# Kernel tuning notes

Measured on AMD Instinct MI355X. Metric: run time of the kernel, lower is better.

The kernel has to match this reference:

```python
import jax, jax.numpy as jnp
import numpy as np

B, T, D = 16, 512, 1024
H = 4
DH = D // H
L = 2
FF = 4 * D
MAX_CORR = 3
THRESH = 0.3
EPS = 1e-5


def _ln(x, g, b):
    mu = x.mean(-1, keepdims=True)
    var = ((x - mu) ** 2).mean(-1, keepdims=True)
    return (x - mu) / jnp.sqrt(var + EPS) * g + b


def _prm(x, Wqkv, bqkv, Wo, bo, ln1_g, ln1_b, W1, b1, W2, b2, ln2_g, ln2_b,
         rh_W1, rh_b1, rh_W2, rh_b2):
    # PyTorch TransformerEncoder (post-LN, relu, dropout off) with causal mask
    Bs, Ts, _ = x.shape
    causal = jnp.triu(jnp.ones((Ts, Ts), dtype=bool), k=1)  # True = masked
    for l in range(L):
        qkv = x @ Wqkv[l].T + bqkv[l]  # (B,T,3D)
        q, k, v = jnp.split(qkv, 3, axis=-1)
        q = q.reshape(Bs, Ts, H, DH)
        k = k.reshape(Bs, Ts, H, DH)
        v = v.reshape(Bs, Ts, H, DH)
        scores = jnp.einsum('bthd,bshd->bhts', q, k) / jnp.sqrt(jnp.float32(DH))
        scores = jnp.where(causal[None, None], -jnp.inf, scores)
        attn = jax.nn.softmax(scores, axis=-1)
        o = jnp.einsum('bhts,bshd->bthd', attn, v).reshape(Bs, Ts, D)
        o = o @ Wo[l].T + bo[l]
        x = _ln(x + o, ln1_g[l], ln1_b[l])
        h = jax.nn.relu(x @ W1[l].T + b1[l]) @ W2[l].T + b2[l]
        x = _ln(x + h, ln2_g[l], ln2_b[l])
    r = jax.nn.relu(x @ rh_W1.T + rh_b1) @ rh_W2.T + rh_b2  # (B,T,1)
    return jax.nn.sigmoid(r[..., 0])  # (B,T)


def setup_inputs() -> dict:
    key = jax.random.key(0)
    ks = jax.random.split(key, 24)
    s = 0.02
    inp = {
        'chain': jax.random.normal(ks[0], (B, T, D), jnp.float32),
        'Wqkv': jax.random.normal(ks[1], (L, 3 * D, D), jnp.float32) * s,
        'bqkv': jnp.zeros((L, 3 * D), jnp.float32),
        'Wo': jax.random.normal(ks[2], (L, D, D), jnp.float32) * s,
        'bo': jnp.zeros((L, D), jnp.float32),
        'ln1_g': jnp.ones((L, D), jnp.float32),
        'ln1_b': jnp.zeros((L, D), jnp.float32),
        'W1': jax.random.normal(ks[3], (L, FF, D), jnp.float32) * s,
        'b1': jnp.zeros((L, FF), jnp.float32),
        'W2': jax.random.normal(ks[4], (L, D, FF), jnp.float32) * s,
        'b2': jnp.zeros((L, D), jnp.float32),
        'ln2_g': jnp.ones((L, D), jnp.float32),
        'ln2_b': jnp.zeros((L, D), jnp.float32),
        'rh_W1': jax.random.normal(ks[5], (D // 2, D), jnp.float32) * s,
        'rh_b1': jnp.zeros((D // 2,), jnp.float32),
        'rh_W2': jax.random.normal(ks[6], (1, D // 2), jnp.float32) * s,
        'rh_b2': jnp.full((1,), -1.0, jnp.float32),  # bias so some scores fall below threshold
        'cor_W1': jax.random.normal(ks[7], (2 * D, 2 * D), jnp.float32) * s,
        'cor_b1': jnp.zeros((2 * D,), jnp.float32),
        'cor_W2': jax.random.normal(ks[8], (D, 2 * D), jnp.float32) * s,
        'cor_b2': jnp.zeros((D,), jnp.float32),
    }
    return inp


def reference(chain, Wqkv, bqkv, Wo, bo, ln1_g, ln1_b, W1, b1, W2, b2,
              ln2_g, ln2_b, rh_W1, rh_b1, rh_W2, rh_b2,
              cor_W1, cor_b1, cor_W2, cor_b2):
    prm = lambda x: _prm(x, Wqkv, bqkv, Wo, bo, ln1_g, ln1_b, W1, b1, W2, b2,
                         ln2_g, ln2_b, rh_W1, rh_b1, rh_W2, rh_b2)
    scores0 = prm(chain)
    corrected = chain
    counts = jnp.zeros((B,), jnp.int32)
    offs = jnp.array([-1, 0, 1], jnp.int32)
    tpos = jnp.arange(T)
    for _ in range(MAX_CORR):
        s = prm(corrected)  # (B,T)
        below = s < THRESH
        has_bad = below.any(axis=-1)  # (B,)
        # worst = first argmin among below-threshold steps (matches torch argmin over gathered)
        w = jnp.argmin(jnp.where(below, s, jnp.inf), axis=-1)  # (B,)
        # context: mean over valid window [w-1, w+2)
        idxs = w[:, None] + offs  # (B,3)
        valid = (idxs >= 0) & (idxs < T)
        gathered = jnp.take_along_axis(corrected, jnp.clip(idxs, 0, T - 1)[..., None], axis=1)  # (B,3,D)
        ctx = (gathered * valid[..., None]).sum(1) / valid.sum(1, keepdims=True)  # (B,D)
        cur = jnp.take_along_axis(corrected, jnp.broadcast_to(w[:, None, None], (B, 1, D)), axis=1)[:, 0]  # (B,D)
        cinp = jnp.concatenate([cur, ctx], axis=-1)  # (B,2D)
        new_step = jax.nn.relu(cinp @ cor_W1.T + cor_b1) @ cor_W2.T + cor_b2  # (B,D)
        sel = (tpos[None, :] == w[:, None]) & has_bad[:, None]  # (B,T)
        corrected = jnp.where(sel[..., None], new_step[:, None, :], corrected)
        counts = counts + has_bad.astype(jnp.int32)
    final_scores = prm(corrected)
    improved = final_scores.mean(-1) > scores0.mean(-1)
    return corrected, counts, final_scores, improved
```

## Files before the change

### kernel.cpp

```cpp
#include <hip/hip_runtime.h>
#include <math.h>

#define B_ 16
#define T_ 512
#define D_ 1024
#define H_ 4
#define DH_ 256
#define FF_ 4096
#define M_ (B_*T_)
#define THRESH_ 0.3f
#define EPS_ 1e-5f

#define GF_RELU 1
#define GF_RES  2
#define GF_OUTBF16 4
#define GF_SPLITV 8

typedef unsigned short ushort_t;
typedef unsigned int uint_t;

using s16x8 = __attribute__((ext_vector_type(8))) short;
using f32x4 = __attribute__((ext_vector_type(4))) float;

typedef const __attribute__((address_space(1))) void* gas_ptr;
typedef __attribute__((address_space(3))) void* lds_ptr;

static __device__ __forceinline__ ushort_t f2bf(float f) {
  uint_t x = __float_as_uint(f);
  return (ushort_t)((x + 0x7FFFu + ((x >> 16) & 1u)) >> 16);
}
static __device__ __forceinline__ float bf2f(ushort_t u) {
  return __uint_as_float(((uint_t)u) << 16);
}

__global__ __launch_bounds__(256)
void cvt_f32_bf16(const float* __restrict__ in, ushort_t* __restrict__ out, int n)
{
  const int i = (blockIdx.x * 256 + threadIdx.x) << 2;
  if (i >= n) return;
  const float4 v = *(const float4*)(in + i);
  ushort4 o;
  o.x = f2bf(v.x); o.y = f2bf(v.y); o.z = f2bf(v.z); o.w = f2bf(v.w);
  *(ushort4*)(out + i) = o;
}

__global__ __launch_bounds__(256)
void gemm_bf16(const ushort_t* __restrict__ A, const ushort_t* __restrict__ Bt,
               const float* __restrict__ bias, const ushort_t* __restrict__ res,
               float* __restrict__ outF, ushort_t* __restrict__ outB,
               ushort_t* __restrict__ vt,
               int M, int N, int K, int flags)
{
  __shared__ ushort_t As[128 * 32];
  __shared__ ushort_t Bs[128 * 32];
  const int n0 = blockIdx.x << 7;
  const int m0 = blockIdx.y << 7;
  const int tid = threadIdx.x;
  const int wv = tid >> 6, ln = tid & 63;
  const int wm = (wv >> 1) << 6;
  const int wn = (wv & 1) << 6;
  const int lrow = ln & 15, quad = ln >> 4;

  f32x4 acc[4][4] = {};

  const ushort_t* ga = A + (size_t)(m0 + wv * 16 + (ln >> 2)) * K + ((ln & 3) << 3);
  const ushort_t* gb = Bt + (size_t)(n0 + wv * 16 + (ln >> 2)) * K + ((ln & 3) << 3);
  ushort_t* lA = &As[wv * 512];
  ushort_t* lB = &Bs[wv * 512];

  for (int k0 = 0; k0 < K; k0 += 32) {
    __builtin_amdgcn_global_load_lds((gas_ptr)(const void*)ga,
                                     (lds_ptr)(void*)lA, 16, 0, 0);
    __builtin_amdgcn_global_load_lds((gas_ptr)(const void*)(ga + (size_t)64 * K),
                                     (lds_ptr)(void*)(lA + 2048), 16, 0, 0);
    __builtin_amdgcn_global_load_lds((gas_ptr)(const void*)gb,
                                     (lds_ptr)(void*)lB, 16, 0, 0);
    __builtin_amdgcn_global_load_lds((gas_ptr)(const void*)(gb + (size_t)64 * K),
                                     (lds_ptr)(void*)(lB + 2048), 16, 0, 0);
    ga += 32; gb += 32;
    __syncthreads();
    s16x8 af[4], bfr[4];
#pragma unroll
    for (int i = 0; i < 4; ++i)
      af[i] = *(const s16x8*)(&As[(wm + i * 16 + lrow) * 32 + quad * 8]);
#pragma unroll
    for (int j = 0; j < 4; ++j)
      bfr[j] = *(const s16x8*)(&Bs[(wn + j * 16 + lrow) * 32 + quad * 8]);
#pragma unroll
    for (int i = 0; i < 4; ++i)
#pragma unroll
      for (int j = 0; j < 4; ++j)
        acc[i][j] = __builtin_amdgcn_mfma_f32_16x16x32_bf16(af[i], bfr[j],
                                                            acc[i][j], 0, 0, 0);
    __syncthreads();
  }

#pragma unroll
  for (int i = 0; i < 4; ++i) {
    const int row0 = m0 + wm + i * 16 + quad * 4;
#pragma unroll
    for (int j = 0; j < 4; ++j) {
      const int c = n0 + wn + j * 16 + lrow;
      const float bb = bias[c];
      const bool isV = (flags & GF_SPLITV) && (c >= 2048);
#pragma unroll
      for (int r = 0; r < 4; ++r) {
        float v = acc[i][j][r] + bb;
        const int m = row0 + r;
        const size_t idx = (size_t)m * N + c;
        if (flags & GF_RES) v += bf2f(res[idx]);
        if (flags & GF_RELU) v = fmaxf(v, 0.f);
        if (isV) {
          const int t = m & 511, bb2 = m >> 9;
          const int hh = (c - 2048) >> 8, d = (c - 2048) & 255;
          vt[(((size_t)(bb2 * 4 + hh) * 16 + (t >> 5)) << 13) + d * 32 + (t & 31)]
              = f2bf(v);
        } else if (flags & GF_OUTBF16) outB[idx] = f2bf(v);
        else outF[idx] = v;
      }
    }
  }
}

__global__ __launch_bounds__(256)
void flash_attn(const ushort_t* __restrict__ qkv, const ushort_t* __restrict__ vtg,
                ushort_t* __restrict__ ao)
{
  __shared__ ushort_t Ks[2][8 * 64 * 32];
  __shared__ ushort_t Vs[2][2 * 256 * 32];
  __shared__ ushort_t Ph[4][16][80];
  __shared__ ushort_t Pl[4][16][80];
  const int qt = (int)gridDim.x - 1 - blockIdx.x;
  const int t0 = qt << 6;
  const int bh = blockIdx.y;
  const int b = bh >> 2, h = bh & 3;
  const int nIter = qt + 1;
  const int tid = threadIdx.x;
  const int wv = tid >> 6, ln = tid & 63;
  const int lrow = ln & 15, quad = ln >> 4;

  s16x8 qf[8];
  {
    const ushort_t* qrow = qkv + (size_t)(b * T_ + t0 + wv * 16 + lrow) * 3072
                           + h * 256 + quad * 8;
#pragma unroll
    for (int kc = 0; kc < 8; ++kc)
      qf[kc] = *(const s16x8*)(qrow + kc * 32);
  }

  const ushort_t* kg = qkv + (size_t)(b * T_) * 3072 + 1024 + h * 256;
  const ushort_t* vg = vtg + (size_t)bh * 131072;

  auto issue_k = [&](int i, int buf) {
#pragma unroll
    for (int iss = 0; iss < 8; ++iss) {
      const int R = 128 * wv + 16 * iss + (ln >> 2);
      const ushort_t* g = kg + (size_t)(64 * i + (R & 63)) * 3072
                          + (R >> 6) * 32 + ((ln & 3) << 3);
      ushort_t* l = &Ks[buf][(128 * wv + 16 * iss) * 32];
      __builtin_amdgcn_global_load_lds((gas_ptr)(const void*)g,
                                       (lds_ptr)(void*)l, 16, 0, 0);
    }
  };
  auto issue_v = [&](int i, int buf) {
#pragma unroll
    for (int iss = 0; iss < 8; ++iss) {
      const ushort_t* g = vg + (size_t)i * 16384 + wv * 4096 + iss * 512 + ln * 8;
      ushort_t* l = &Vs[buf][wv * 4096 + iss * 512];
      __builtin_amdgcn_global_load_lds((gas_ptr)(const void*)g,
                                       (lds_ptr)(void*)l, 16, 0, 0);
    }
  };

  issue_k(0, 0);
  issue_v(0, 0);

  f32x4 o[16] = {};
  float Mx[4], L[4];
#pragma unroll
  for (int r = 0; r < 4; ++r) { Mx[r] = -3.0e38f; L[r] = 0.f; }

  for (int it = 0; it < nIter; ++it) {
    const int buf = it & 1;
    __syncthreads();
    if (it + 1 < nIter) { issue_k(it + 1, buf ^ 1); issue_v(it + 1, buf ^ 1); }

    f32x4 s[4] = {};
#pragma unroll
    for (int kc = 0; kc < 8; ++kc)
#pragma unroll
      for (int j = 0; j < 4; ++j) {
        const s16x8 bfv = *(const s16x8*)(&Ks[buf][(kc * 64 + 16 * j + lrow) * 32
                                                   + quad * 8]);
        s[j] = __builtin_amdgcn_mfma_f32_16x16x32_bf16(qf[kc], bfv, s[j], 0, 0, 0);
      }

    const bool diag = (it == qt);
#pragma unroll
    for (int j = 0; j < 4; ++j)
#pragma unroll
      for (int r = 0; r < 4; ++r) {
        float v = s[j][r] * 0.0625f;
        if (diag && (16 * j + lrow > 16 * wv + quad * 4 + r)) v = -INFINITY;
        s[j][r] = v;
      }

    float alpha[4];
#pragma unroll
    for (int r = 0; r < 4; ++r) {
      float m = fmaxf(fmaxf(s[0][r], s[1][r]), fmaxf(s[2][r], s[3][r]));
      m = fmaxf(m, __shfl_xor(m, 1));
      m = fmaxf(m, __shfl_xor(m, 2));
      m = fmaxf(m, __shfl_xor(m, 4));
      m = fmaxf(m, __shfl_xor(m, 8));
      const float mn = fmaxf(Mx[r], m);
      alpha[r] = __expf(Mx[r] - mn);
      Mx[r] = mn;
      float l = 0.f;
#pragma unroll
      for (int j = 0; j < 4; ++j) {
        const float p = __expf(s[j][r] - mn);
        s[j][r] = p;
        l += p;
      }
      l += __shfl_xor(l, 1);
      l += __shfl_xor(l, 2);
      l += __shfl_xor(l, 4);
      l += __shfl_xor(l, 8);
      L[r] = L[r] * alpha[r] + l;
    }

#pragma unroll
    for (int j = 0; j < 4; ++j)
#pragma unroll
      for (int r = 0; r < 4; ++r) {
        const float p = s[j][r];
        const ushort_t hi = f2bf(p);
        Ph[wv][quad * 4 + r][16 * j + lrow] = hi;
        Pl[wv][quad * 4 + r][16 * j + lrow] = f2bf(p - bf2f(hi));
      }
#pragma unroll
    for (int jd = 0; jd < 16; ++jd)
#pragma unroll
      for (int r = 0; r < 4; ++r)
        o[jd][r] *= alpha[r];

#pragma unroll
    for (int c = 0; c < 2; ++c) {
      const s16x8 ph = *(const s16x8*)(&Ph[wv][lrow][32 * c + quad * 8]);
      const s16x8 pl = *(const s16x8*)(&Pl[wv][lrow][32 * c + quad * 8]);
#pragma unroll
      for (int jd = 0; jd < 16; ++jd) {
        const s16x8 vb = *(const s16x8*)(&Vs[buf][(c * 256 + 16 * jd + lrow) * 32
                                                  + quad * 8]);
        o[jd] = __builtin_amdgcn_mfma_f32_16x16x32_bf16(ph, vb, o[jd], 0, 0, 0);
        o[jd] = __builtin_amdgcn_mfma_f32_16x16x32_bf16(pl, vb, o[jd], 0, 0, 0);
      }
    }
  }

  float inv[4];
#pragma unroll
  for (int r = 0; r < 4; ++r) inv[r] = 1.f / L[r];
  ushort_t* aob = ao + (size_t)(b * T_ + t0 + 16 * wv + quad * 4) * 1024 + h * 256;
#pragma unroll
  for (int jd = 0; jd < 16; ++jd)
#pragma unroll
    for (int r = 0; r < 4; ++r)
      aob[(size_t)r * 1024 + 16 * jd + lrow] = f2bf(o[jd][r] * inv[r]);
}

__global__ __launch_bounds__(256)
void gemm_bt(const float* __restrict__ A, const float* __restrict__ Bt,
             const float* __restrict__ bias, float* __restrict__ out,
             int M, int N, int K, int flags)
{
  __shared__ float As[16][68];
  __shared__ float Bs[16][68];
  const int n0 = blockIdx.x << 6;
  const int m0 = blockIdx.y << 6;
  const int tx = threadIdx.x, ty = threadIdx.y;
  const int tid = (ty << 4) + tx;
  const int lr = tid >> 2;
  const int lc = (tid & 3) << 2;
  float c[4][4] = {};
  for (int k0 = 0; k0 < K; k0 += 16) {
    float4 av = make_float4(0.f, 0.f, 0.f, 0.f);
    if (m0 + lr < M)
      av = *(const float4*)(A + (size_t)(m0 + lr) * K + k0 + lc);
    const float4 bv = *(const float4*)(Bt + (size_t)(n0 + lr) * K + k0 + lc);
    As[lc + 0][lr] = av.x; As[lc + 1][lr] = av.y;
    As[lc + 2][lr] = av.z; As[lc + 3][lr] = av.w;
    Bs[lc + 0][lr] = bv.x; Bs[lc + 1][lr] = bv.y;
    Bs[lc + 2][lr] = bv.z; Bs[lc + 3][lr] = bv.w;
    __syncthreads();
#pragma unroll
    for (int k = 0; k < 16; ++k) {
      const float4 a = *(const float4*)(&As[k][ty << 2]);
      const float4 b = *(const float4*)(&Bs[k][tx << 2]);
      c[0][0] += a.x*b.x; c[0][1] += a.x*b.y; c[0][2] += a.x*b.z; c[0][3] += a.x*b.w;
      c[1][0] += a.y*b.x; c[1][1] += a.y*b.y; c[1][2] += a.y*b.z; c[1][3] += a.y*b.w;
      c[2][0] += a.z*b.x; c[2][1] += a.z*b.y; c[2][2] += a.z*b.z; c[2][3] += a.z*b.w;
      c[3][0] += a.w*b.x; c[3][1] += a.w*b.y; c[3][2] += a.w*b.z; c[3][3] += a.w*b.w;
    }
    __syncthreads();
  }
  const int n = n0 + (tx << 2);
  const float4 bb = *(const float4*)(bias + n);
#pragma unroll
  for (int i = 0; i < 4; ++i) {
    const int m = m0 + (ty << 2) + i;
    if (m >= M) break;
    float4 v = make_float4(c[i][0] + bb.x, c[i][1] + bb.y,
                           c[i][2] + bb.z, c[i][3] + bb.w);
    if (flags & GF_RELU) {
      v.x = fmaxf(v.x, 0.f); v.y = fmaxf(v.y, 0.f);
      v.z = fmaxf(v.z, 0.f); v.w = fmaxf(v.w, 0.f);
    }
    *(float4*)(out + (size_t)m * N + n) = v;
  }
}

__global__ __launch_bounds__(256)
void layernorm_k(const float* __restrict__ in, const float* __restrict__ g,
                 const float* __restrict__ bta, ushort_t* __restrict__ outb)
{
  const int row = blockIdx.x;
  const int tid = threadIdx.x;
  const int wave = tid >> 6, lane = tid & 63;
  const float4 v = *(const float4*)(in + (size_t)row * D_ + (tid << 2));
  float s = v.x + v.y + v.z + v.w;
  float ss = v.x*v.x + v.y*v.y + v.z*v.z + v.w*v.w;
  for (int off = 32; off; off >>= 1) {
    s  += __shfl_down(s, off, 64);
    ss += __shfl_down(ss, off, 64);
  }
  __shared__ float ra[4], rb[4];
  if (!lane) { ra[wave] = s; rb[wave] = ss; }
  __syncthreads();
  s  = ra[0] + ra[1] + ra[2] + ra[3];
  ss = rb[0] + rb[1] + rb[2] + rb[3];
  const float mu = s * (1.f / (float)D_);
  const float var = ss * (1.f / (float)D_) - mu * mu;
  const float rstd = rsqrtf(var + EPS_);
  const float4 gv = *(const float4*)(g + (tid << 2));
  const float4 bv = *(const float4*)(bta + (tid << 2));
  ushort4 o;
  o.x = f2bf((v.x - mu) * rstd * gv.x + bv.x);
  o.y = f2bf((v.y - mu) * rstd * gv.y + bv.y);
  o.z = f2bf((v.z - mu) * rstd * gv.z + bv.z);
  o.w = f2bf((v.w - mu) * rstd * gv.w + bv.w);
  *(ushort4*)(outb + (size_t)row * D_ + (tid << 2)) = o;
}

__global__ __launch_bounds__(256)
void head2_sigmoid(const float* __restrict__ h1, const float* __restrict__ w2,
                   const float* __restrict__ b2, float* __restrict__ sout)
{
  const int tid = threadIdx.x;
  const int wave = tid >> 6, lane = tid & 63;
  const int m = (blockIdx.x << 2) + wave;
  const float* hr = h1 + (size_t)m * 512;
  float s = 0.f;
#pragma unroll
  for (int i = 0; i < 8; ++i) s += hr[i * 64 + lane] * w2[i * 64 + lane];
  for (int off = 32; off; off >>= 1) s += __shfl_down(s, off, 64);
  if (!lane) sout[m] = 1.f / (1.f + expf(-(s + b2[0])));
}

__global__ __launch_bounds__(256)
void select_worst(const float* __restrict__ s, int* __restrict__ w,
                  int* __restrict__ hasbad, int* __restrict__ counts)
{
  const int b = blockIdx.x, tid = threadIdx.x;
  const float* sr = s + b * T_;
  float bv = INFINITY; int bi = 0;
  for (int i = tid; i < T_; i += 256) {
    const float v = sr[i];
    const float cand = (v < THRESH_) ? v : INFINITY;
    if (cand < bv || (cand == bv && i < bi)) { bv = cand; bi = i; }
  }
  __shared__ float rv[256];
  __shared__ int ri[256];
  rv[tid] = bv; ri[tid] = bi;
  __syncthreads();
  for (int str = 128; str; str >>= 1) {
    if (tid < str) {
      const float v2 = rv[tid + str]; const int i2 = ri[tid + str];
      if (v2 < rv[tid] || (v2 == rv[tid] && i2 < ri[tid])) { rv[tid] = v2; ri[tid] = i2; }
    }
    __syncthreads();
  }
  if (!tid) {
    const int bad = (rv[0] < INFINITY) ? 1 : 0;
    w[b] = ri[0];
    hasbad[b] = bad;
    counts[b] += bad;
  }
}

__global__ __launch_bounds__(256)
void gather_cinp(const float* __restrict__ corr, const int* __restrict__ w,
                 float* __restrict__ cinp)
{
  const int b = blockIdx.x, tid = threadIdx.x;
  const int wi = w[b];
  const float* base = corr + (size_t)b * T_ * D_;
  const int nv = 3 - (wi == 0 ? 1 : 0) - (wi == T_ - 1 ? 1 : 0);
  const float inv = 1.f / (float)nv;
  const int d = tid << 2;
  const float4 cur = *(const float4*)(base + (size_t)wi * D_ + d);
  float4 acc = cur;
  if (wi > 0) {
    const float4 p = *(const float4*)(base + (size_t)(wi - 1) * D_ + d);
    acc.x += p.x; acc.y += p.y; acc.z += p.z; acc.w += p.w;
  }
  if (wi < T_ - 1) {
    const float4 p = *(const float4*)(base + (size_t)(wi + 1) * D_ + d);
    acc.x += p.x; acc.y += p.y; acc.z += p.z; acc.w += p.w;
  }
  acc.x *= inv; acc.y *= inv; acc.z *= inv; acc.w *= inv;
  *(float4*)(cinp + (size_t)b * (2 * D_) + d) = cur;
  *(float4*)(cinp + (size_t)b * (2 * D_) + D_ + d) = acc;
}

__global__ __launch_bounds__(256)
void apply_corr(float* __restrict__ corr, const int* __restrict__ w,
                const int* __restrict__ hasbad, const float* __restrict__ ns)
{
  const int b = blockIdx.x;
  if (!hasbad[b]) return;
  const int wi = w[b], tid = threadIdx.x;
  *(float4*)(corr + (size_t)(b * T_ + wi) * D_ + (tid << 2)) =
      *(const float4*)(ns + (size_t)b * D_ + (tid << 2));
}

__global__ __launch_bounds__(256)
void init_copy(const float* __restrict__ chain, float* __restrict__ corr,
               int* __restrict__ counts)
{
  const size_t i = ((size_t)blockIdx.x * 256 + threadIdx.x) << 2;
  *(float4*)(corr + i) = *(const float4*)(chain + i);
  if (blockIdx.x == 0 && threadIdx.x < B_) counts[threadIdx.x] = 0;
}

__global__ __launch_bounds__(256)
void finalize_k(const float* __restrict__ s0, const float* __restrict__ fs,
                const int* __restrict__ cnt, float* __restrict__ oc,
                float* __restrict__ oi)
{
  const int b = blockIdx.x, tid = threadIdx.x;
  const int wave = tid >> 6, lane = tid & 63;
  float a = s0[b * T_ + tid] + s0[b * T_ + tid + 256];
  float c = fs[b * T_ + tid] + fs[b * T_ + tid + 256];
  for (int off = 32; off; off >>= 1) {
    a += __shfl_down(a, off, 64);
    c += __shfl_down(c, off, 64);
  }
  __shared__ float ra[4], rc[4];
  if (!lane) { ra[wave] = a; rc[wave] = c; }
  __syncthreads();
  if (!tid) {
    const float as = ra[0] + ra[1] + ra[2] + ra[3];
    const float cs = rc[0] + rc[1] + rc[2] + rc[3];
    oc[b] = (float)cnt[b];
    oi[b] = (cs > as) ? 1.f : 0.f;
  }
}

extern "C" void kernel_launch(void* const* d_in, const int* in_sizes, int n_in,
                              void* d_out, int out_size, void* d_ws, size_t ws_size,
                              hipStream_t stream)
{
  const float* chain  = (const float*)d_in[0];
  const float* Wqkv   = (const float*)d_in[1];
  const float* bqkv   = (const float*)d_in[2];
  const float* Wo     = (const float*)d_in[3];
  const float* bo     = (const float*)d_in[4];
  const float* ln1g   = (const float*)d_in[5];
  const float* ln1b   = (const float*)d_in[6];
  const float* W1     = (const float*)d_in[7];
  const float* b1     = (const float*)d_in[8];
  const float* W2     = (const float*)d_in[9];
  const float* b2     = (const float*)d_in[10];
  const float* ln2g   = (const float*)d_in[11];
  const float* ln2b   = (const float*)d_in[12];
  const float* rhW1   = (const float*)d_in[13];
  const float* rhb1   = (const float*)d_in[14];
  const float* rhW2   = (const float*)d_in[15];
  const float* rhb2   = (const float*)d_in[16];
  const float* corW1  = (const float*)d_in[17];
  const float* corb1  = (const float*)d_in[18];
  const float* corW2  = (const float*)d_in[19];
  const float* corb2  = (const float*)d_in[20];

  float* ws = (float*)d_ws;
  ushort_t* QKV16 = (ushort_t*)ws;
  float*    PRE   = ws;
  float*    E     = ws;
  ushort_t* Hb    = (ushort_t*)(ws + 12582912);
  ushort_t* Vtg   = (ushort_t*)(ws + 12582912);
  ushort_t* Xb    = (ushort_t*)(ws + 29360128);
  ushort_t* AOb   = (ushort_t*)(ws + 33554432);
  float*    HH    = ws + 33554432;
  float*    cinp  = ws + 33554432;
  float*    corrH = cinp + 32768;
  float*    nstep = corrH + 32768;
  ushort_t* W16     = (ushort_t*)(ws + 37748736);
  ushort_t* Wqkv16  = W16;
  ushort_t* Wo16    = W16 + 6291456;
  ushort_t* W116    = W16 + 8388608;
  ushort_t* W216    = W16 + 16777216;
  ushort_t* rhW116  = W16 + 25165824;
  float* s0buf = ws + 50593792;
  float* sbuf  = s0buf + 8192;
  int* wbuf   = (int*)(sbuf + 8192);
  int* badbuf = wbuf + 16;
  int* cntbuf = badbuf + 16;

  float* outCorr   = (float*)d_out;
  float* outCounts = outCorr + 8388608;
  float* outFS     = outCounts + 16;
  float* outImpr   = outFS + 8192;

  const dim3 blk2(16, 16);
  const dim3 blk1(256);

  cvt_f32_bf16<<<dim3(6144), blk1, 0, stream>>>(Wqkv, Wqkv16, 6291456);
  cvt_f32_bf16<<<dim3(2048), blk1, 0, stream>>>(Wo,   Wo16,   2097152);
  cvt_f32_bf16<<<dim3(8192), blk1, 0, stream>>>(W1,   W116,   8388608);
  cvt_f32_bf16<<<dim3(8192), blk1, 0, stream>>>(W2,   W216,   8388608);
  cvt_f32_bf16<<<dim3(512),  blk1, 0, stream>>>(rhW1, rhW116, 524288);

  auto run_prm = [&](const float* xin, float* scoresOut) {
    cvt_f32_bf16<<<dim3(8192), blk1, 0, stream>>>(xin, Xb, 8388608);
    for (int l = 0; l < 2; ++l) {
      gemm_bf16<<<dim3(24, 64), blk1, 0, stream>>>(
          Xb, Wqkv16 + (size_t)l * 3 * D_ * D_, bqkv + (size_t)l * 3 * D_,
          nullptr, nullptr, QKV16, Vtg, M_, 3 * D_, D_,
          GF_OUTBF16 | GF_SPLITV);
      flash_attn<<<dim3(8, 64), blk1, 0, stream>>>(QKV16, Vtg, AOb);
      gemm_bf16<<<dim3(8, 64), blk1, 0, stream>>>(
          AOb, Wo16 + (size_t)l * D_ * D_, bo + (size_t)l * D_,
          Xb, PRE, nullptr, nullptr, M_, D_, D_, GF_RES);
      layernorm_k<<<dim3(M_), blk1, 0, stream>>>(PRE, ln1g + l * D_,
                                                 ln1b + l * D_, Xb);
      gemm_bf16<<<dim3(32, 64), blk1, 0, stream>>>(
          Xb, W116 + (size_t)l * FF_ * D_, b1 + (size_t)l * FF_,
          nullptr, nullptr, Hb, nullptr, M_, FF_, D_, GF_RELU | GF_OUTBF16);
      gemm_bf16<<<dim3(8, 64), blk1, 0, stream>>>(
          Hb, W216 + (size_t)l * D_ * FF_, b2 + (size_t)l * D_,
          Xb, E, nullptr, nullptr, M_, D_, FF_, GF_RES);
      layernorm_k<<<dim3(M_), blk1, 0, stream>>>(E, ln2g + l * D_,
                                                 ln2b + l * D_, Xb);
    }
    gemm_bf16<<<dim3(4, 64), blk1, 0, stream>>>(
        Xb, rhW116, rhb1, nullptr, HH, nullptr, nullptr, M_, 512, D_, GF_RELU);
    head2_sigmoid<<<dim3(M_ / 4), blk1, 0, stream>>>(HH, rhW2, rhb2, scoresOut);
  };

  auto run_iter = [&](const float* sPtr) {
    select_worst<<<dim3(B_), blk1, 0, stream>>>(sPtr, wbuf, badbuf, cntbuf);
    gather_cinp<<<dim3(B_), blk1, 0, stream>>>(outCorr, wbuf, cinp);
    gemm_bt<<<dim3(32, 1), blk2, 0, stream>>>(cinp, corW1, corb1, corrH,
                                              B_, 2 * D_, 2 * D_, GF_RELU);
    gemm_bt<<<dim3(16, 1), blk2, 0, stream>>>(corrH, corW2, corb2, nstep,
                                              B_, D_, 2 * D_, 0);
    apply_corr<<<dim3(B_), blk1, 0, stream>>>(outCorr, wbuf, badbuf, nstep);
  };

  init_copy<<<dim3(8192), blk1, 0, stream>>>(chain, outCorr, cntbuf);

  run_prm(chain, s0buf);
  run_iter(s0buf);
  run_prm(outCorr, sbuf);
  run_iter(sbuf);
  run_prm(outCorr, sbuf);
  run_iter(sbuf);
  run_prm(outCorr, outFS);
  finalize_k<<<dim3(B_), blk1, 0, stream>>>(s0buf, outFS, cntbuf,
                                            outCounts, outImpr);
  (void)in_sizes; (void)n_in; (void)out_size; (void)ws_size;
}
```

Before: 5.237 ms.

## Use 32x32x16 MFMA tiles and grouped block swizzle in bf16 GEMM

Switches the GEMM inner loop from 16x16x32 MFMA to 32x32x16 MFMA instructions, with each wave computing a 2x2 grid of 32x32 tiles instead of 4x4 of 16x16. This reduces LDS fragment reads per MFMA and uses the larger MFMA shape. It also remaps block IDs into groups of 8 M-tiles so neighbouring blocks share B/A panels in L2. The epilogue row mapping changes to the 32x32 accumulator layout, which adds a correctness risk if that mapping is wrong.

```diff
diff --git a/kernel.cpp b/kernel.cpp
--- a/kernel.cpp
+++ b/kernel.cpp
@@ -21,6 +21,7 @@
 
 using s16x8 = __attribute__((ext_vector_type(8))) short;
 using f32x4 = __attribute__((ext_vector_type(4))) float;
+using f32x16 = __attribute__((ext_vector_type(16))) float;
 
 typedef const __attribute__((address_space(1))) void* gas_ptr;
 typedef __attribute__((address_space(3))) void* lds_ptr;
@@ -53,15 +54,22 @@
 {
   __shared__ ushort_t As[128 * 32];
   __shared__ ushort_t Bs[128 * 32];
-  const int n0 = blockIdx.x << 7;
-  const int m0 = blockIdx.y << 7;
+  const int npn = gridDim.x;
+  const int pid = blockIdx.y * npn + blockIdx.x;
+  const int group = 8 * npn;
+  const int first_m = (pid / group) * 8;
+  const int pid_m = first_m + (pid % 8);
+  const int pid_n = (pid % group) >> 3;
+  const int n0 = pid_n << 7;
+  const int m0 = pid_m << 7;
+
   const int tid = threadIdx.x;
   const int wv = tid >> 6, ln = tid & 63;
   const int wm = (wv >> 1) << 6;
   const int wn = (wv & 1) << 6;
-  const int lrow = ln & 15, quad = ln >> 4;
-
-  f32x4 acc[4][4] = {};
+  const int col32 = ln & 31, l5 = ln >> 5;
+
+  f32x16 acc[2][2] = {};
 
   const ushort_t* ga = A + (size_t)(m0 + wv * 16 + (ln >> 2)) * K + ((ln & 3) << 3);
   const ushort_t* gb = Bt + (size_t)(n0 + wv * 16 + (ln >> 2)) * K + ((ln & 3) << 3);
@@ -79,39 +87,47 @@
                                      (lds_ptr)(void*)(lB + 2048), 16, 0, 0);
     ga += 32; gb += 32;
     __syncthreads();
-    s16x8 af[4], bfr[4];
-#pragma unroll
-    for (int i = 0; i < 4; ++i)
-      af[i] = *(const s16x8*)(&As[(wm + i * 16 + lrow) * 32 + quad * 8]);
-#pragma unroll
-    for (int j = 0; j < 4; ++j)
-      bfr[j] = *(const s16x8*)(&Bs[(wn + j * 16 + lrow) * 32 + quad * 8]);
-#pragma unroll
-    for (int i = 0; i < 4; ++i)
-#pragma unroll
-      for (int j = 0; j < 4; ++j)
-        acc[i][j] = __builtin_amdgcn_mfma_f32_16x16x32_bf16(af[i], bfr[j],
-                                                            acc[i][j], 0, 0, 0);
+    s16x8 af[2][2], bfr[2][2];
+#pragma unroll
+    for (int mt = 0; mt < 2; ++mt)
+#pragma unroll
+      for (int kh = 0; kh < 2; ++kh)
+        af[mt][kh] = *(const s16x8*)(&As[(wm + mt * 32 + col32) * 32
+                                         + kh * 16 + l5 * 8]);
+#pragma unroll
+    for (int nt = 0; nt < 2; ++nt)
+#pragma unroll
+      for (int kh = 0; kh < 2; ++kh)
+        bfr[nt][kh] = *(const s16x8*)(&Bs[(wn + nt * 32 + col32) * 32
+                                          + kh * 16 + l5 * 8]);
+#pragma unroll
+    for (int kh = 0; kh < 2; ++kh)
+#pragma unroll
+      for (int mt = 0; mt < 2; ++mt)
+#pragma unroll
+        for (int nt = 0; nt < 2; ++nt)
+          acc[mt][nt] = __builtin_amdgcn_mfma_f32_32x32x16_bf16(
+              af[mt][kh], bfr[nt][kh], acc[mt][nt], 0, 0, 0);
     __syncthreads();
   }
 
 #pragma unroll
-  for (int i = 0; i < 4; ++i) {
-    const int row0 = m0 + wm + i * 16 + quad * 4;
-#pragma unroll
-    for (int j = 0; j < 4; ++j) {
-      const int c = n0 + wn + j * 16 + lrow;
+  for (int mt = 0; mt < 2; ++mt)
+#pragma unroll
+    for (int nt = 0; nt < 2; ++nt) {
+      const int c = n0 + wn + nt * 32 + col32;
       const float bb = bias[c];
       const bool isV = (flags & GF_SPLITV) && (c >= 2048);
 #pragma unroll
-      for (int r = 0; r < 4; ++r) {
-        float v = acc[i][j][r] + bb;
-        const int m = row0 + r;
-        const size_t idx = (size_t)m * N + c;
+      for (int reg = 0; reg < 16; ++reg) {
+        const int row = m0 + wm + mt * 32 + (reg & 3) + ((reg >> 2) << 3)
+                        + (l5 << 2);
+        float v = acc[mt][nt][reg] + bb;
+        const size_t idx = (size_t)row * N + c;
         if (flags & GF_RES) v += bf2f(res[idx]);
         if (flags & GF_RELU) v = fmaxf(v, 0.f);
         if (isV) {
-          const int t = m & 511, bb2 = m >> 9;
+          const int t = row & 511, bb2 = row >> 9;
           const int hh = (c - 2048) >> 8, d = (c - 2048) & 255;
           vt[(((size_t)(bb2 * 4 + hh) * 16 + (t >> 5)) << 13) + d * 32 + (t & 31)]
               = f2bf(v);
@@ -119,7 +135,6 @@
         else outF[idx] = v;
       }
     }
-  }
 }
 
 __global__ __launch_bounds__(256)
```

Measured after the change: 5.136 ms. No clear change (-1.9%).
